# Optimization experiments

Measured on AMD Instinct MI355X. Metric: run time of the kernel, lower is better.

The kernel has to match this reference:

```python
import jax, jax.numpy as jnp
import numpy as np

ALPHA = 2.0  # spikingjelly surrogate.Erf default alpha

@jax.custom_vjp
def erf_spike(x):
    # spiking forward: heaviside(x); backward uses Erf surrogate gradient
    return (x >= 0).astype(x.dtype)

def _erf_spike_fwd(x):
    return erf_spike(x), x

def _erf_spike_bwd(x, g):
    return (g * jnp.exp(-(x * ALPHA) ** 2) * (ALPHA / np.sqrt(np.pi)),)

erf_spike.defvjp(_erf_spike_fwd, _erf_spike_bwd)

L, T, B, C, H, N_LAYERS = 256, 4, 32, 256, 256, 2

def setup_inputs() -> dict:
    key = jax.random.key(0)
    ks = jax.random.split(key, 8)
    k = 1.0 / np.sqrt(H)  # uniform(-sqrt(1/H), sqrt(1/H)) init
    u = lambda kk, shape: jax.random.uniform(kk, shape, jnp.float32, -k, k)
    return {
        "x": jax.random.normal(ks[0], (L, T, B, C), jnp.float32),
        "W_ih0": u(ks[1], (4 * H, C)),
        "W_hh0": u(ks[2], (4 * H, H)),
        "b0": u(ks[3], (4 * H,)),
        "W_ih1": u(ks[4], (4 * H, H)),
        "W_hh1": u(ks[5], (4 * H, H)),
        "b1": u(ks[6], (4 * H,)),
    }

def _run_layer(inp, W_ih, W_hh, b):
    # inp: [L, T, B, Cin] -> fold T,B into one batch axis for the scan
    Ls, Ts, Bs = inp.shape[0], inp.shape[1], inp.shape[2]
    Hs = W_hh.shape[1]
    xin = inp.reshape(Ls, Ts * Bs, -1)

    def step(carry, x_t):
        h, c = carry
        gates = x_t @ W_ih.T + h @ W_hh.T + b  # [TB, 4H]
        i, f, g, o = jnp.split(gates, 4, axis=-1)
        i = erf_spike(i)
        f = erf_spike(f)
        g = erf_spike(g)
        o = erf_spike(o)
        c = f * c + i * g
        # torch.clamp_max_ under no_grad: value clamp, straight-through grad
        c = c + jax.lax.stop_gradient(jnp.minimum(c, 1.0) - c)
        h = o * c
        return (h, c), h

    h0 = jnp.zeros((Ts * Bs, Hs), inp.dtype)
    (h, c), out = jax.lax.scan(step, (h0, h0), xin)
    return (out.reshape(Ls, Ts, Bs, Hs),
            h.reshape(Ts, Bs, Hs),
            c.reshape(Ts, Bs, Hs))

def reference(x, W_ih0, W_hh0, b0, W_ih1, W_hh1, b1):
    out0, h0, c0 = _run_layer(x, W_ih0, W_hh0, b0)
    out1, h1, c1 = _run_layer(out0, W_ih1, W_hh1, b1)
    state_h = jnp.stack([h0, h1])  # [N, T, B, H]
    state_c = jnp.stack([c0, c1])
    return out1, (state_h, state_c)
```

## Files before the change

kernel.cpp:

```cpp
#include <hip/hip_runtime.h>
#include <math.h>

typedef _Float16 half8 __attribute__((ext_vector_type(8)));
typedef _Float16 half4v __attribute__((ext_vector_type(4)));
typedef float floatx4 __attribute__((ext_vector_type(4)));
typedef unsigned long long u64;

#define MFMA16(a, b, c) __builtin_amdgcn_mfma_f32_16x16x32_f16((a), (b), (c), 0, 0, 0)
#define AARG __ATOMIC_RELAXED, __HIP_MEMORY_SCOPE_AGENT

static constexpr float C11 = 4.8828125e-4f;
static constexpr int SLOTS = 257;
static constexpr int LSTRIDE = SLOTS * 8 * 128;

__device__ u64 g_exch[2 * LSTRIDE];
__device__ _Float16 g_xhi[8388608];
__device__ _Float16 g_xlo[8388608];
__device__ float g_phi[33554432];
__device__ _Float16 g_plo[33554432];

__device__ __forceinline__ u64 ald(const u64* p) { return __hip_atomic_load(p, AARG); }
__device__ __forceinline__ void ast(u64* p, u64 v) { __hip_atomic_store(p, v, AARG); }

__device__ __forceinline__ void barrier_lds() {
  __builtin_amdgcn_sched_barrier(0);
  asm volatile("s_waitcnt lgkmcnt(0)" ::: "memory");
  __builtin_amdgcn_s_barrier();
  __builtin_amdgcn_sched_barrier(0);
}

__device__ __forceinline__ void split16(float v, _Float16& hi, _Float16& lo) {
  _Float16 h = (fabsf(v) < 6.103515625e-05f) ? (_Float16)0.0f : (_Float16)v;
  hi = h;
  lo = (_Float16)((v - (float)h) * 2048.0f);
}

__global__ __launch_bounds__(256) void presplit_k(const float* __restrict__ x) {
  unsigned gi = blockIdx.x * 256 + threadIdx.x;
  if (gi < 2 * LSTRIDE) g_exch[gi] = 0;
  int i = (int)gi * 8;
  floatx4 a = *(const floatx4*)(x + i);
  floatx4 b = *(const floatx4*)(x + i + 4);
  half8 hi, lo;
#pragma unroll
  for (int e = 0; e < 4; ++e) { _Float16 p, q; split16(a[e], p, q); hi[e] = p; lo[e] = q; }
#pragma unroll
  for (int e = 0; e < 4; ++e) { _Float16 p, q; split16(b[e], p, q); hi[4 + e] = p; lo[4 + e] = q; }
  *(half8*)(g_xhi + i) = hi;
  *(half8*)(g_xlo + i) = lo;
}

__global__ __launch_bounds__(256) void gemm0_k(const float* __restrict__ wih) {
  const int tid = threadIdx.x, lane = tid & 63, wv = tid >> 6;
  const int m16 = lane & 15, l16 = lane >> 4;
  const int bi = blockIdx.x;
  const int lc = bi >> 6, g = (bi >> 3) & 7, kwg = bi & 7;

  half8 WH[2][8], WL[2][8];
#pragma unroll
  for (int t2 = 0; t2 < 2; ++t2) {
    int grow = wv * 256 + 32 * kwg + t2 * 16 + m16;
#pragma unroll
    for (int q = 0; q < 8; ++q) {
      const float* src = wih + (size_t)grow * 256 + 32 * q + 8 * l16;
      floatx4 v0 = *(const floatx4*)src;
      floatx4 v1 = *(const floatx4*)(src + 4);
      half8 hi, lo;
#pragma unroll
      for (int e = 0; e < 4; ++e) { _Float16 p, q2; split16(v0[e], p, q2); hi[e] = p; lo[e] = q2; }
#pragma unroll
      for (int e = 0; e < 4; ++e) { _Float16 p, q2; split16(v1[e], p, q2); hi[4 + e] = p; lo[4 + e] = q2; }
      WH[t2][q] = hi;
      WL[t2][q] = lo;
    }
  }
#pragma unroll 1
  for (int l = lc * 32; l < lc * 32 + 32; ++l) {
    size_t base = ((size_t)l * 128 + 16 * g + m16) * 256 + 8 * l16;
    half8 xh[8], xl[8];
#pragma unroll
    for (int q = 0; q < 8; ++q) {
      xh[q] = *(const half8*)(g_xhi + base + 32 * q);
      xl[q] = *(const half8*)(g_xlo + base + 32 * q);
    }
    floatx4 zz = {0.f, 0.f, 0.f, 0.f};
    floatx4 A0[2], A1[2], A2[2];
    A0[0] = A0[1] = zz; A1[0] = A1[1] = zz; A2[0] = A2[1] = zz;
#pragma unroll
    for (int q = 0; q < 8; ++q)
#pragma unroll
      for (int t2 = 0; t2 < 2; ++t2) {
        A0[t2] = MFMA16(xh[q], WH[t2][q], A0[t2]);
        A1[t2] = MFMA16(xh[q], WL[t2][q], A1[t2]);
        A1[t2] = MFMA16(xl[q], WH[t2][q], A1[t2]);
        A2[t2] = MFMA16(xl[q], WL[t2][q], A2[t2]);
      }
#pragma unroll
    for (int t2 = 0; t2 < 2; ++t2) {
      size_t off = ((((((size_t)l * 8 + g) * 8 + kwg) * 4 + wv) * 2 + t2) * 64 + lane) * 4;
      *(floatx4*)(g_phi + off) = A0[t2];
      half4v hv;
#pragma unroll
      for (int r = 0; r < 4; ++r) hv[r] = (_Float16)(A1[t2][r] + C11 * A2[t2][r]);
      *(half4v*)(g_plo + off) = hv;
    }
  }
}

template <int LAYER>
__device__ void scan_body(_Float16* lut, float* ihb, unsigned* hw, u64* spike,
                          const float* __restrict__ wih,
                          const float* __restrict__ whh,
                          const float* __restrict__ bias,
                          float* __restrict__ dout, int g, int kwg) {
  const int tid = threadIdx.x;
  const int lane = tid & 63;
  const int wv = tid >> 6;
  const bool prod = wv < 4;
  const int gate = wv & 3;
  const int m16 = lane & 15;
  const int l16 = lane >> 4;

  u64* exch0 = g_exch;
  u64* exchMy = g_exch + LAYER * LSTRIDE;

  if (tid < 256) {
#pragma unroll
    for (int e = 0; e < 8; ++e)
      lut[tid * 8 + e] = ((tid >> e) & 1) ? (_Float16)1.0f : (_Float16)0.0f;
  }

  half8 FH[2][8], FL[2][8];
  if (!prod || LAYER == 1) {
    const float* wsrc = prod ? wih : whh;
#pragma unroll
    for (int t2 = 0; t2 < 2; ++t2) {
      int grow = gate * 256 + 32 * kwg + t2 * 16 + m16;
#pragma unroll
      for (int q = 0; q < 8; ++q) {
        const float* src = wsrc + (size_t)grow * 256 + 32 * q + 8 * l16;
        floatx4 v0 = *(const floatx4*)src;
        floatx4 v1 = *(const floatx4*)(src + 4);
        half8 hi, lo;
#pragma unroll
        for (int e = 0; e < 4; ++e) { _Float16 p, q2; split16(v0[e], p, q2); hi[e] = p; lo[e] = q2; }
#pragma unroll
        for (int e = 0; e < 4; ++e) { _Float16 p, q2; split16(v1[e], p, q2); hi[4 + e] = p; lo[4 + e] = q2; }
        FH[t2][q] = hi;
        FL[t2][q] = lo;
      }
    }
  }
  float bl[2];
#pragma unroll
  for (int t2 = 0; t2 < 2; ++t2) bl[t2] = bias[gate * 256 + 32 * kwg + t2 * 16 + m16];

  floatx4 ihA0[2], ihA1[2];
  floatx4 phv[2];
  half4v plv[2];
  u64 xwA[8];
  unsigned xw[8];
  u64 cst = 0;
  int polls = 0;
  const int POLL_MAX = 1 << 22;

  auto issue_pl = [&](int l) {
#pragma unroll
    for (int t2 = 0; t2 < 2; ++t2) {
      size_t off = ((((((size_t)l * 8 + g) * 8 + kwg) * 4 + gate) * 2 + t2) * 64 + lane) * 4;
      phv[t2] = *(const floatx4*)(g_phi + off);
      plv[t2] = *(const half4v*)(g_plo + off);
    }
  };
  auto issue_xw = [&](int tag) {
    const u64* page = exch0 + (size_t)tag * 1024 + g * 128 + m16;
#pragma unroll
    for (int q = 0; q < 8; ++q) xwA[q] = ald(page + q * 16);
  };
  auto consume_xw = [&](int tag) {
    bool ok = true;
#pragma unroll
    for (int q = 0; q < 8; ++q) ok = ok && ((unsigned)xwA[q] == (unsigned)tag);
    if (!__all(ok)) {
      const u64* page = exch0 + (size_t)tag * 1024 + g * 128 + m16;
      for (;;) {
#pragma unroll
        for (int q = 0; q < 8; ++q) xwA[q] = ald(page + q * 16);
        bool k2 = true;
#pragma unroll
        for (int q = 0; q < 8; ++q) k2 = k2 && ((unsigned)xwA[q] == (unsigned)tag);
        if (__all(k2)) break;
        if (++polls > POLL_MAX) break;
      }
    }
#pragma unroll
    for (int q = 0; q < 8; ++q) xw[q] = (unsigned)(xwA[q] >> 32);
  };
  auto ih_mfma = [&]() {
    floatx4 zz = {0.f, 0.f, 0.f, 0.f};
    ihA0[0] = ihA0[1] = zz;
    ihA1[0] = ihA1[1] = zz;
#pragma unroll
    for (int q = 0; q < 8; ++q) {
      unsigned byt = (xw[q] >> (8 * l16)) & 0xFFu;
      half8 ah = *(const half8*)(lut + byt * 8);
#pragma unroll
      for (int t2 = 0; t2 < 2; ++t2) {
        ihA0[t2] = MFMA16(ah, FH[t2][q], ihA0[t2]);
        ihA1[t2] = MFMA16(ah, FL[t2][q], ihA1[t2]);
      }
    }
  };
  auto gather16 = [&](u64 v) -> unsigned {
    unsigned a0 = __shfl((unsigned)v, lane & 3);
    unsigned a1 = __shfl((unsigned)(v >> 32), lane & 3);
    unsigned b0 = __shfl((unsigned)v, 4 + (lane & 3));
    unsigned b1 = __shfl((unsigned)(v >> 32), 4 + (lane & 3));
    u64 A = ((u64)a1 << 32) | a0;
    u64 B = ((u64)b1 << 32) | b0;
    int sh = 16 * ((lane & 15) >> 2);
    return (unsigned)((A >> sh) & 0xFFFFull) |
           ((unsigned)((B >> sh) & 0xFFFFull) << 16);
  };

  if (prod) {
    if constexpr (LAYER == 0) {
      issue_pl(0);
    } else {
      issue_xw(1);
      consume_xw(1);
      ih_mfma();
      issue_xw(2);
    }
  }
  __syncthreads();

#pragma unroll 1
  for (int l = 0; l < 256; ++l) {
    if (prod) {
#pragma unroll
      for (int t2 = 0; t2 < 2; ++t2) {
        float* b2 = ihb + ((gate * 2 + t2) * 8) * 64 + lane;
        if constexpr (LAYER == 0) {
#pragma unroll
          for (int r = 0; r < 4; ++r) {
            b2[r * 64] = phv[t2][r];
            b2[(4 + r) * 64] = (float)plv[t2][r];
          }
        } else {
#pragma unroll
          for (int r = 0; r < 4; ++r) {
            b2[r * 64] = ihA0[t2][r];
            b2[(4 + r) * 64] = ihA1[t2][r];
          }
        }
      }
    } else if (wv == 4 && l > 0) {
      const u64* pa = exchMy + (size_t)l * 1024 + g * 128 + 2 * lane;
      u64 v0 = ald(pa), v1 = ald(pa + 1);
      for (;;) {
        if (__all(((unsigned)v0 == (unsigned)l) && ((unsigned)v1 == (unsigned)l))) break;
        v0 = ald(pa);
        v1 = ald(pa + 1);
        if (++polls > POLL_MAX) break;
      }
      hw[2 * lane] = (unsigned)(v0 >> 32);
      hw[2 * lane + 1] = (unsigned)(v1 >> 32);
    }
    barrier_lds();
    if (prod) {
      if (l < 255) {
        if constexpr (LAYER == 0) {
          issue_pl(l + 1);
        } else {
          consume_xw(l + 2);
          ih_mfma();
          if (l + 3 <= 256) issue_xw(l + 3);
        }
      }
    } else {
      floatx4 C0[2], C1[2];
#pragma unroll
      for (int t2 = 0; t2 < 2; ++t2) {
        const float* b2 = ihb + ((gate * 2 + t2) * 8) * 64 + lane;
#pragma unroll
        for (int r = 0; r < 4; ++r) {
          C0[t2][r] = b2[r * 64];
          C1[t2][r] = b2[(4 + r) * 64];
        }
      }
      if (l > 0) {
#pragma unroll
        for (int q = 0; q < 8; ++q) {
          unsigned mw = hw[q * 16 + m16];
          unsigned byt = (mw >> (8 * l16)) & 0xFFu;
          half8 af = *(const half8*)(lut + byt * 8);
          C0[0] = MFMA16(af, FH[0][q], C0[0]);
          C0[1] = MFMA16(af, FH[1][q], C0[1]);
          C1[0] = MFMA16(af, FL[0][q], C1[0]);
          C1[1] = MFMA16(af, FL[1][q], C1[1]);
        }
      }
      u64 bal[2][4];
#pragma unroll
      for (int r = 0; r < 4; ++r) {
        float p0 = C0[0][r] + bl[0] + C11 * C1[0][r];
        float p1 = C0[1][r] + bl[1] + C11 * C1[1][r];
        bal[0][r] = __ballot(p0 >= 0.0f);
        bal[1][r] = __ballot(p1 >= 0.0f);
      }
      if (lane == 0) {
#pragma unroll
        for (int t2 = 0; t2 < 2; ++t2)
#pragma unroll
          for (int r = 0; r < 4; ++r) spike[gate * 8 + t2 * 4 + r] = bal[t2][r];
      }
    }
    barrier_lds();
    {
      int idx = lane & 7;
      u64 iS = spike[idx], fS = spike[8 + idx];
      u64 gS = spike[16 + idx];
      cst = (fS & cst) | (iS & gS);
    }
    u64 hS = spike[24 + (lane & 7)] & cst;
    if (wv == 0) {
      unsigned hu = gather16(hS);
      if (lane < 16)
        ast(exchMy + (size_t)(l + 1) * 1024 + g * 128 + kwg * 16 + lane,
            ((u64)hu << 32) | (unsigned)(l + 1));
    }
    if (LAYER == 1 && wv == 1) {
      unsigned hu = gather16(hS);
      if (lane < 16) {
        float* frow = dout + ((size_t)l * 128 + 16 * g + lane) * 256 + 32 * kwg;
#pragma unroll
        for (int c4 = 0; c4 < 8; ++c4) {
          floatx4 v;
#pragma unroll
          for (int j = 0; j < 4; ++j) v[j] = ((hu >> (c4 * 4 + j)) & 1) ? 1.0f : 0.0f;
          *(floatx4*)(frow + c4 * 4) = v;
        }
      }
    }
    if (l == 255 && wv == 2) {
      unsigned hu = gather16(hS);
      unsigned cu = gather16(cst);
      if (lane < 16) {
        float* shp = dout + 8388608 + LAYER * 32768 +
                     (size_t)(16 * g + lane) * 256 + 32 * kwg;
        float* scp = shp + 65536;
#pragma unroll
        for (int c4 = 0; c4 < 8; ++c4) {
          floatx4 vh, vc;
#pragma unroll
          for (int j = 0; j < 4; ++j) {
            vh[j] = ((hu >> (c4 * 4 + j)) & 1) ? 1.0f : 0.0f;
            vc[j] = ((cu >> (c4 * 4 + j)) & 1) ? 1.0f : 0.0f;
          }
          *(floatx4*)(shp + c4 * 4) = vh;
          *(floatx4*)(scp + c4 * 4) = vc;
        }
      }
    }
  }
}

__global__ __launch_bounds__(512, 2) void spike_scan(
    const float* __restrict__ wih1, const float* __restrict__ whh0,
    const float* __restrict__ whh1, const float* __restrict__ b0,
    const float* __restrict__ b1, float* __restrict__ dout) {
  __shared__ __align__(16) _Float16 lut[256 * 8];
  __shared__ __align__(16) float ihb[4 * 2 * 8 * 64];
  __shared__ unsigned hw[128];
  __shared__ u64 spike[32];

  int bi = blockIdx.x;
  int g = bi & 7;
  int kwg = (bi >> 3) & 7;
  if ((bi >> 6) == 0)
    scan_body<0>(lut, ihb, hw, spike, (const float*)nullptr, whh0, b0, dout, g, kwg);
  else
    scan_body<1>(lut, ihb, hw, spike, wih1, whh1, b1, dout, g, kwg);
}

extern "C" void kernel_launch(void* const* d_in, const int* in_sizes, int n_in,
                              void* d_out, int out_size, void* d_ws, size_t ws_size,
                              hipStream_t stream) {
  (void)in_sizes; (void)n_in; (void)out_size; (void)d_ws; (void)ws_size;
  const float* x = (const float*)d_in[0];
  const float* wih0 = (const float*)d_in[1];
  const float* whh0 = (const float*)d_in[2];
  const float* b0 = (const float*)d_in[3];
  const float* wih1 = (const float*)d_in[4];
  const float* whh1 = (const float*)d_in[5];
  const float* b1 = (const float*)d_in[6];
  float* dout = (float*)d_out;

  presplit_k<<<4096, 256, 0, stream>>>(x);
  gemm0_k<<<512, 256, 0, stream>>>(wih0);
  spike_scan<<<128, 512, 0, stream>>>(wih1, whh0, whh1, b0, b1, dout);
}
```

Measured before the change: 624.6 us.

## Interleave gate rows so each lane holds all four gates, drop second barrier

Reorders the recurrent weight rows so each consumer lane's MFMA output holds the i/f/g/o gate values for the same hidden unit. The cell update then runs in registers per lane instead of through ballots stored to shared memory and a second block barrier. The ih buffer and h-word buffer are double-buffered by step parity, with padded strides, so one barrier per step is enough. The transposed MFMA operand order and the lane-to-element remapping add index arithmetic and risk subtle mapping bugs.

```diff
diff --git a/kernel.cpp b/kernel.cpp
--- a/kernel.cpp
+++ b/kernel.cpp
@@ -12,6 +12,8 @@
 static constexpr float C11 = 4.8828125e-4f;
 static constexpr int SLOTS = 257;
 static constexpr int LSTRIDE = SLOTS * 8 * 128;
+static constexpr int IHP = 4 * 32 * 17;
+static constexpr int IHB = 2 * IHP;
 
 __device__ u64 g_exch[2 * LSTRIDE];
 __device__ _Float16 g_xhi[8388608];
@@ -108,7 +110,7 @@
 }
 
 template <int LAYER>
-__device__ void scan_body(_Float16* lut, float* ihb, unsigned* hw, u64* spike,
+__device__ void scan_body(_Float16* lut, float* ihb, unsigned* hw,
                           const float* __restrict__ wih,
                           const float* __restrict__ whh,
                           const float* __restrict__ bias,
@@ -118,8 +120,11 @@
   const int wv = tid >> 6;
   const bool prod = wv < 4;
   const int gate = wv & 3;
+  const int wl = wv & 3;
   const int m16 = lane & 15;
   const int l16 = lane >> 4;
+  const int jk = lane >> 4;
+  const int sq = lane & 15;
 
   u64* exch0 = g_exch;
   u64* exchMy = g_exch + LAYER * LSTRIDE;
@@ -131,14 +136,13 @@
   }
 
   half8 FH[2][8], FL[2][8];
-  if (!prod || LAYER == 1) {
-    const float* wsrc = prod ? wih : whh;
+  if (!prod) {
 #pragma unroll
     for (int t2 = 0; t2 < 2; ++t2) {
-      int grow = gate * 256 + 32 * kwg + t2 * 16 + m16;
+      int grow = (m16 & 3) * 256 + 32 * kwg + 8 * wl + 4 * t2 + (m16 >> 2);
 #pragma unroll
       for (int q = 0; q < 8; ++q) {
-        const float* src = wsrc + (size_t)grow * 256 + 32 * q + 8 * l16;
+        const float* src = whh + (size_t)grow * 256 + 32 * q + 8 * l16;
         floatx4 v0 = *(const floatx4*)src;
         floatx4 v1 = *(const floatx4*)(src + 4);
         half8 hi, lo;
@@ -150,17 +154,40 @@
         FL[t2][q] = lo;
       }
     }
-  }
-  float bl[2];
-#pragma unroll
-  for (int t2 = 0; t2 < 2; ++t2) bl[t2] = bias[gate * 256 + 32 * kwg + t2 * 16 + m16];
+  } else if (LAYER == 1) {
+#pragma unroll
+    for (int t2 = 0; t2 < 2; ++t2) {
+      int grow = gate * 256 + 32 * kwg + t2 * 16 + m16;
+#pragma unroll
+      for (int q = 0; q < 8; ++q) {
+        const float* src = wih + (size_t)grow * 256 + 32 * q + 8 * l16;
+        floatx4 v0 = *(const floatx4*)src;
+        floatx4 v1 = *(const floatx4*)(src + 4);
+        half8 hi, lo;
+#pragma unroll
+        for (int e = 0; e < 4; ++e) { _Float16 p, q2; split16(v0[e], p, q2); hi[e] = p; lo[e] = q2; }
+#pragma unroll
+        for (int e = 0; e < 4; ++e) { _Float16 p, q2; split16(v1[e], p, q2); hi[4 + e] = p; lo[4 + e] = q2; }
+        FH[t2][q] = hi;
+        FL[t2][q] = lo;
+      }
+    }
+  }
+  float blv[2][4];
+  if (!prod) {
+#pragma unroll
+    for (int t2 = 0; t2 < 2; ++t2)
+#pragma unroll
+      for (int r = 0; r < 4; ++r)
+        blv[t2][r] = bias[r * 256 + 32 * kwg + 8 * wl + 4 * t2 + jk];
+  }
 
   floatx4 ihA0[2], ihA1[2];
   floatx4 phv[2];
   half4v plv[2];
   u64 xwA[8];
   unsigned xw[8];
-  u64 cst = 0;
+  int cA = 0, cB = 0;
   int polls = 0;
   const int POLL_MAX = 1 << 22;
 
@@ -173,7 +200,7 @@
     }
   };
   auto issue_xw = [&](int tag) {
-    const u64* page = exch0 + (size_t)tag * 1024 + g * 128 + m16;
+    const u64* page = exch0 + (size_t)tag * 1024 + g * 128 + l16 * 4 + (m16 >> 2);
 #pragma unroll
     for (int q = 0; q < 8; ++q) xwA[q] = ald(page + q * 16);
   };
@@ -182,7 +209,7 @@
 #pragma unroll
     for (int q = 0; q < 8; ++q) ok = ok && ((unsigned)xwA[q] == (unsigned)tag);
     if (!__all(ok)) {
-      const u64* page = exch0 + (size_t)tag * 1024 + g * 128 + m16;
+      const u64* page = exch0 + (size_t)tag * 1024 + g * 128 + l16 * 4 + (m16 >> 2);
       for (;;) {
 #pragma unroll
         for (int q = 0; q < 8; ++q) xwA[q] = ald(page + q * 16);
@@ -202,7 +229,7 @@
     ihA1[0] = ihA1[1] = zz;
 #pragma unroll
     for (int q = 0; q < 8; ++q) {
-      unsigned byt = (xw[q] >> (8 * l16)) & 0xFFu;
+      unsigned byt = (xw[q] >> (8 * (m16 & 3))) & 0xFFu;
       half8 ah = *(const half8*)(lut + byt * 8);
 #pragma unroll
       for (int t2 = 0; t2 < 2; ++t2) {
@@ -211,17 +238,8 @@
       }
     }
   };
-  auto gather16 = [&](u64 v) -> unsigned {
-    unsigned a0 = __shfl((unsigned)v, lane & 3);
-    unsigned a1 = __shfl((unsigned)(v >> 32), lane & 3);
-    unsigned b0 = __shfl((unsigned)v, 4 + (lane & 3));
-    unsigned b1 = __shfl((unsigned)(v >> 32), 4 + (lane & 3));
-    u64 A = ((u64)a1 << 32) | a0;
-    u64 B = ((u64)b1 << 32) | b0;
-    int sh = 16 * ((lane & 15) >> 2);
-    return (unsigned)((A >> sh) & 0xFFFFull) |
-           ((unsigned)((B >> sh) & 0xFFFFull) << 16);
-  };
+
+  __syncthreads();
 
   if (prod) {
     if constexpr (LAYER == 0) {
@@ -233,28 +251,24 @@
       issue_xw(2);
     }
   }
-  __syncthreads();
 
 #pragma unroll 1
   for (int l = 0; l < 256; ++l) {
     if (prod) {
-#pragma unroll
-      for (int t2 = 0; t2 < 2; ++t2) {
-        float* b2 = ihb + ((gate * 2 + t2) * 8) * 64 + lane;
-        if constexpr (LAYER == 0) {
-#pragma unroll
-          for (int r = 0; r < 4; ++r) {
-            b2[r * 64] = phv[t2][r];
-            b2[(4 + r) * 64] = (float)plv[t2][r];
-          }
-        } else {
-#pragma unroll
-          for (int r = 0; r < 4; ++r) {
-            b2[r * 64] = ihA0[t2][r];
-            b2[(4 + r) * 64] = ihA1[t2][r];
+      float* ib = ihb + (l & 1) * IHB;
+#pragma unroll
+      for (int t2 = 0; t2 < 2; ++t2)
+#pragma unroll
+        for (int r = 0; r < 4; ++r) {
+          int idx = (gate * 32 + t2 * 16 + l16 * 4 + r) * 17 + m16;
+          if constexpr (LAYER == 0) {
+            ib[idx] = phv[t2][r];
+            ib[IHP + idx] = (float)plv[t2][r];
+          } else {
+            ib[idx] = ihA0[t2][r];
+            ib[IHP + idx] = ihA1[t2][r];
           }
         }
-      }
     } else if (wv == 4 && l > 0) {
       const u64* pa = exchMy + (size_t)l * 1024 + g * 128 + 2 * lane;
       u64 v0 = ald(pa), v1 = ald(pa + 1);
@@ -264,8 +278,9 @@
         v1 = ald(pa + 1);
         if (++polls > POLL_MAX) break;
       }
-      hw[2 * lane] = (unsigned)(v0 >> 32);
-      hw[2 * lane + 1] = (unsigned)(v1 >> 32);
+      unsigned* hwb = hw + (l & 1) * 128;
+      hwb[2 * lane] = (unsigned)(v0 >> 32);
+      hwb[2 * lane + 1] = (unsigned)(v1 >> 32);
     }
     barrier_lds();
     if (prod) {
@@ -279,88 +294,77 @@
         }
       }
     } else {
+      const float* ib = ihb + (l & 1) * IHB;
       floatx4 C0[2], C1[2];
 #pragma unroll
       for (int t2 = 0; t2 < 2; ++t2) {
-        const float* b2 = ihb + ((gate * 2 + t2) * 8) * 64 + lane;
+        int jrel = 8 * wl + 4 * t2 + jk;
 #pragma unroll
         for (int r = 0; r < 4; ++r) {
-          C0[t2][r] = b2[r * 64];
-          C1[t2][r] = b2[(4 + r) * 64];
+          int idx = (r * 32 + (jrel >> 4) * 16 + sq) * 17 + (jrel & 15);
+          C0[t2][r] = ib[idx];
+          C1[t2][r] = ib[IHP + idx];
         }
       }
       if (l > 0) {
+        const unsigned* hwb = hw + (l & 1) * 128;
 #pragma unroll
         for (int q = 0; q < 8; ++q) {
-          unsigned mw = hw[q * 16 + m16];
-          unsigned byt = (mw >> (8 * l16)) & 0xFFu;
-          half8 af = *(const half8*)(lut + byt * 8);
-          C0[0] = MFMA16(af, FH[0][q], C0[0]);
-          C0[1] = MFMA16(af, FH[1][q], C0[1]);
-          C1[0] = MFMA16(af, FL[0][q], C1[0]);
-          C1[1] = MFMA16(af, FL[1][q], C1[1]);
+          unsigned word = hwb[q * 16 + jk * 4 + (sq >> 2)];
+          unsigned byt = (word >> (8 * (sq & 3))) & 0xFFu;
+          half8 bf = *(const half8*)(lut + byt * 8);
+          C0[0] = MFMA16(FH[0][q], bf, C0[0]);
+          C0[1] = MFMA16(FH[1][q], bf, C0[1]);
+          C1[0] = MFMA16(FL[0][q], bf, C1[0]);
+          C1[1] = MFMA16(FL[1][q], bf, C1[1]);
         }
       }
-      u64 bal[2][4];
-#pragma unroll
-      for (int r = 0; r < 4; ++r) {
-        float p0 = C0[0][r] + bl[0] + C11 * C1[0][r];
-        float p1 = C0[1][r] + bl[1] + C11 * C1[1][r];
-        bal[0][r] = __ballot(p0 >= 0.0f);
-        bal[1][r] = __ballot(p1 >= 0.0f);
-      }
-      if (lane == 0) {
-#pragma unroll
-        for (int t2 = 0; t2 < 2; ++t2)
-#pragma unroll
-          for (int r = 0; r < 4; ++r) spike[gate * 8 + t2 * 4 + r] = bal[t2][r];
-      }
-    }
-    barrier_lds();
-    {
-      int idx = lane & 7;
-      u64 iS = spike[idx], fS = spike[8 + idx];
-      u64 gS = spike[16 + idx];
-      cst = (fS & cst) | (iS & gS);
-    }
-    u64 hS = spike[24 + (lane & 7)] & cst;
-    if (wv == 0) {
-      unsigned hu = gather16(hS);
-      if (lane < 16)
-        ast(exchMy + (size_t)(l + 1) * 1024 + g * 128 + kwg * 16 + lane,
-            ((u64)hu << 32) | (unsigned)(l + 1));
-    }
-    if (LAYER == 1 && wv == 1) {
-      unsigned hu = gather16(hS);
-      if (lane < 16) {
-        float* frow = dout + ((size_t)l * 128 + 16 * g + lane) * 256 + 32 * kwg;
-#pragma unroll
-        for (int c4 = 0; c4 < 8; ++c4) {
-          floatx4 v;
-#pragma unroll
-          for (int j = 0; j < 4; ++j) v[j] = ((hu >> (c4 * 4 + j)) & 1) ? 1.0f : 0.0f;
-          *(floatx4*)(frow + c4 * 4) = v;
-        }
-      }
-    }
-    if (l == 255 && wv == 2) {
-      unsigned hu = gather16(hS);
-      unsigned cu = gather16(cst);
-      if (lane < 16) {
+      int iA = (C0[0][0] + blv[0][0] + C11 * C1[0][0]) >= 0.0f;
+      int fA = (C0[0][1] + blv[0][1] + C11 * C1[0][1]) >= 0.0f;
+      int gA = (C0[0][2] + blv[0][2] + C11 * C1[0][2]) >= 0.0f;
+      int oA = (C0[0][3] + blv[0][3] + C11 * C1[0][3]) >= 0.0f;
+      int iB = (C0[1][0] + blv[1][0] + C11 * C1[1][0]) >= 0.0f;
+      int fB = (C0[1][1] + blv[1][1] + C11 * C1[1][1]) >= 0.0f;
+      int gB = (C0[1][2] + blv[1][2] + C11 * C1[1][2]) >= 0.0f;
+      int oB = (C0[1][3] + blv[1][3] + C11 * C1[1][3]) >= 0.0f;
+      cA = (fA & cA) | (iA & gA);
+      cB = (fB & cB) | (iB & gB);
+      int hA = oA & cA;
+      int hB = oB & cB;
+      u64 balA = __ballot(hA != 0);
+      u64 balB = __ballot(hB != 0);
+      unsigned pb = (unsigned)((balA >> sq) & 1) |
+                    ((unsigned)((balA >> (16 + sq)) & 1) << 1) |
+                    ((unsigned)((balA >> (32 + sq)) & 1) << 2) |
+                    ((unsigned)((balA >> (48 + sq)) & 1) << 3) |
+                    ((unsigned)((balB >> sq) & 1) << 4) |
+                    ((unsigned)((balB >> (16 + sq)) & 1) << 5) |
+                    ((unsigned)((balB >> (32 + sq)) & 1) << 6) |
+                    ((unsigned)((balB >> (48 + sq)) & 1) << 7);
+      int bse = 4 * (lane & 3);
+      unsigned q0 = __shfl(pb, bse);
+      unsigned q1 = __shfl(pb, bse + 1);
+      unsigned q2 = __shfl(pb, bse + 2);
+      unsigned q3 = __shfl(pb, bse + 3);
+      if (lane < 4) {
+        u64 atom = ((u64)(q0 | (q1 << 8) | (q2 << 16) | (q3 << 24)) << 32) |
+                   (unsigned)(l + 1);
+        ast(exchMy + (size_t)(l + 1) * 1024 + g * 128 + kwg * 16 + wl * 4 + lane,
+            atom);
+      }
+      if constexpr (LAYER == 1) {
+        float* frow = dout + ((size_t)l * 128 + 16 * g + sq) * 256 + 32 * kwg + 8 * wl;
+        frow[jk] = hA ? 1.0f : 0.0f;
+        frow[4 + jk] = hB ? 1.0f : 0.0f;
+      }
+      if (l == 255) {
         float* shp = dout + 8388608 + LAYER * 32768 +
-                     (size_t)(16 * g + lane) * 256 + 32 * kwg;
+                     (size_t)(16 * g + sq) * 256 + 32 * kwg + 8 * wl;
         float* scp = shp + 65536;
-#pragma unroll
-        for (int c4 = 0; c4 < 8; ++c4) {
-          floatx4 vh, vc;
-#pragma unroll
-          for (int j = 0; j < 4; ++j) {
-            vh[j] = ((hu >> (c4 * 4 + j)) & 1) ? 1.0f : 0.0f;
-            vc[j] = ((cu >> (c4 * 4 + j)) & 1) ? 1.0f : 0.0f;
-          }
-          *(floatx4*)(shp + c4 * 4) = vh;
-          *(floatx4*)(scp + c4 * 4) = vc;
-        }
+        shp[jk] = hA ? 1.0f : 0.0f;
+        shp[4 + jk] = hB ? 1.0f : 0.0f;
+        scp[jk] = cA ? 1.0f : 0.0f;
+        scp[4 + jk] = cB ? 1.0f : 0.0f;
       }
     }
   }
@@ -371,17 +375,16 @@
     const float* __restrict__ whh1, const float* __restrict__ b0,
     const float* __restrict__ b1, float* __restrict__ dout) {
   __shared__ __align__(16) _Float16 lut[256 * 8];
-  __shared__ __align__(16) float ihb[4 * 2 * 8 * 64];
-  __shared__ unsigned hw[128];
-  __shared__ u64 spike[32];
+  __shared__ __align__(16) float ihb[2 * IHB];
+  __shared__ unsigned hw[2 * 128];
 
   int bi = blockIdx.x;
   int g = bi & 7;
   int kwg = (bi >> 3) & 7;
   if ((bi >> 6) == 0)
-    scan_body<0>(lut, ihb, hw, spike, (const float*)nullptr, whh0, b0, dout, g, kwg);
+    scan_body<0>(lut, ihb, hw, (const float*)nullptr, whh0, b0, dout, g, kwg);
   else
-    scan_body<1>(lut, ihb, hw, spike, wih1, whh1, b1, dout, g, kwg);
+    scan_body<1>(lut, ihb, hw, wih1, whh1, b1, dout, g, kwg);
 }
 
 extern "C" void kernel_launch(void* const* d_in, const int* in_sizes, int n_in,
```

Result: slower. 647.9 us (+3.7%).
